# Performance work log

Hardware: AMD Instinct MI355X
Metric: run time of the kernel (lower is better)

## Reference

```python
import jax, jax.numpy as jnp
import numpy as np
import math

P = 2
TAU = 1.0
USE_POW = False
ALIGN_W = 1.0
ENTROPY_W = 1.0
EPS = 1e-12


def _pairwise_l2(z):
    # torch.cdist(z, z, p=2): sqrt of squared distances via GEMM decomposition
    sq = jnp.sum(z * z, axis=-1)  # [N]
    d2 = sq[:, None] + sq[None, :] - 2.0 * (z @ z.T)  # [N, N]
    d = jnp.sqrt(jnp.maximum(d2, 0.0))
    return jnp.maximum(d, EPS)  # clamp_min(eps)


def setup_inputs() -> dict:
    key = jax.random.key(0)
    k0, k1 = jax.random.split(key)
    v0 = jax.random.normal(k0, (8192, 256), dtype=jnp.float32)
    v1 = jax.random.normal(k1, (8192, 256), dtype=jnp.float32)
    return {"v0": v0, "v1": v1}


def reference(v0, v1):
    views = [v0, v1]
    n = v0.shape[0]

    # Alignment term: mean Lp distance between matched rows, one pair (0,1)
    diff = v0 - v1
    align = jnp.sqrt(jnp.sum(diff * diff, axis=-1)).mean()  # p=2 norm per row

    # Entropy term: masked logsumexp over within-view pairwise distances
    log_num_neg = math.log(n - 1)
    eye = jnp.eye(n, dtype=bool)
    entropy = jnp.float32(0.0)
    for z in views:
        dist = _pairwise_l2(z)  # [N, N]
        logits = jnp.where(eye, -jnp.inf, -dist / TAU)
        lme = jax.nn.logsumexp(logits, axis=1) - log_num_neg  # [N]
        entropy = entropy + lme.mean()
    entropy = entropy / len(views)

    return ALIGN_W * align + ENTROPY_W * entropy
```

## Files before the change

kernel.cpp:

```cpp
#include <hip/hip_runtime.h>
#include <math.h>


#define D_DIM 256
#define NB 64
#define NSEG 544
#define S_Q 26.0f
#define LOG2E2 2.0813689810f
#define LP 65

typedef int i32x4 __attribute__((ext_vector_type(4)));
typedef unsigned int u32;
#define AS1 __attribute__((address_space(1)))
#define AS3 __attribute__((address_space(3)))

__device__ inline void load_lds16(const void* g, void* l) {
  __builtin_amdgcn_global_load_lds((const AS1 u32*)g, (AS3 u32*)l, 16, 0, 0);
}

__device__ inline int q8(float x) {
  return __float2int_rn(fminf(fmaxf(x * S_Q, -127.0f), 127.0f));
}
__device__ inline u32 q8x4(const float4 f) {
  return (u32)(q8(f.x) & 255) | ((u32)(q8(f.y) & 255) << 8) |
         ((u32)(q8(f.z) & 255) << 16) | ((u32)(q8(f.w) & 255) << 24);
}

__device__ inline int G4fun(int M) {
  const int m = M >> 2, r = M & 3;
  return 2 * m * (m + 1) + r * (m + 1);
}

__global__ __launch_bounds__(256) void prep(
    const float* __restrict__ v0, const float* __restrict__ v1,
    unsigned char* __restrict__ ph0, unsigned char* __restrict__ ph1,
    float* __restrict__ sq0, float* __restrict__ sq1,
    float* __restrict__ S0, float* __restrict__ S1,
    float* __restrict__ align_part,
    double* __restrict__ totals, int* __restrict__ ticket) {
  __shared__ float4 l0[16 * LP], l1[16 * LP];
  __shared__ float red0[4][16], red1[4][16], red2[4][16];
  const int R = blockIdx.x;
  const int t = threadIdx.x;

  if (R == 0 && t == 0) { totals[0] = 0.0; totals[1] = 0.0; ticket[0] = 0; }

  #pragma unroll
  for (int p = 0; p < 4; ++p) {
    const int slot = t + p * 256;
    const int r = slot >> 6, col = slot & 63;
    const size_t g = (size_t)(R * 16 + r) * 64 + col;
    l0[r * LP + col] = ((const float4*)v0)[g];
    l1[r * LP + col] = ((const float4*)v1)[g];
  }
  __syncthreads();

  {
    const int rr = t & 15, c = t >> 4;
    const int s = c >> 2, q = c & 3;
    const int li = rr * LP + c * 4;
    uint4 u0, u1;
    u0.x = q8x4(l0[li + 0]); u0.y = q8x4(l0[li + 1]);
    u0.z = q8x4(l0[li + 2]); u0.w = q8x4(l0[li + 3]);
    u1.x = q8x4(l1[li + 0]); u1.y = q8x4(l1[li + 1]);
    u1.z = q8x4(l1[li + 2]); u1.w = q8x4(l1[li + 3]);
    const size_t dst = (size_t)(R * 4 + s) * 64 + q * 16 + rr;
    ((uint4*)ph0)[dst] = u0;
    ((uint4*)ph1)[dst] = u1;
  }

  {
    const int rr = t & 15;
    const int base = rr * LP + (t >> 4) * 4;
    float s0p = 0.f, s1p = 0.f, s2p = 0.f;
    #pragma unroll
    for (int c = 0; c < 4; ++c) {
      const float4 a = l0[base + c], b = l1[base + c];
      s0p += a.x * a.x + a.y * a.y + a.z * a.z + a.w * a.w;
      s1p += b.x * b.x + b.y * b.y + b.z * b.z + b.w * b.w;
      const float dx = a.x - b.x, dy = a.y - b.y, dz = a.z - b.z, dw = a.w - b.w;
      s2p += dx * dx + dy * dy + dz * dz + dw * dw;
    }
    s0p += __shfl_xor(s0p, 16, 64); s0p += __shfl_xor(s0p, 32, 64);
    s1p += __shfl_xor(s1p, 16, 64); s1p += __shfl_xor(s1p, 32, 64);
    s2p += __shfl_xor(s2p, 16, 64); s2p += __shfl_xor(s2p, 32, 64);
    const int w = t >> 6, lane = t & 63;
    if (lane < 16) { red0[w][lane] = s0p; red1[w][lane] = s1p; red2[w][lane] = s2p; }
  }
  __syncthreads();
  if (t < 16) {
    const int row = R * 16 + t;
    const float a0 = red0[0][t] + red0[1][t] + red0[2][t] + red0[3][t];
    const float a1 = red1[0][t] + red1[1][t] + red1[2][t] + red1[3][t];
    const float a2 = red2[0][t] + red2[1][t] + red2[2][t] + red2[3][t];
    sq0[row] = a0 * LOG2E2;
    sq1[row] = a1 * LOG2E2;
    align_part[row] = sqrtf(a2);
    S0[row] = 0.0f;
    S1[row] = 0.0f;
  }
}

__global__ __launch_bounds__(256) void entropy_tile(
    const unsigned char* __restrict__ ph0, const unsigned char* __restrict__ ph1,
    const float* __restrict__ sq0, const float* __restrict__ sq1,
    float* __restrict__ S0, float* __restrict__ S1) {
  const unsigned char* __restrict__ ph = blockIdx.y ? ph1 : ph0;
  const float* __restrict__ sq = blockIdx.y ? sq1 : sq0;
  float* __restrict__ S        = blockIdx.y ? S1 : S0;

  const int lin = blockIdx.x;
  int bi = 0;
  while (NSEG - G4fun(64 - (bi + 1)) <= lin) ++bi;
  const int q = lin - (NSEG - G4fun(64 - bi));
  const int bj0 = bi + 4 * q;
  const int jend = (bj0 + 3 < NB - 1) ? bj0 + 3 : NB - 1;

  __shared__ __align__(16) char smem[32768];
  float* swp = (float*)smem;

  const int t = threadIdx.x, lane = t & 63, w = t >> 6;
  const int wi = w >> 1, wj = w & 1;
  const int quad = lane >> 4, l15 = lane & 15;
  const int i0 = bi * 128;

  #pragma unroll
  for (int r8 = 0; r8 < 8; ++r8) {
    const int seg = w * 8 + r8;
    const unsigned char* src = ph + (size_t)bi * 32768 + seg * 1024 + lane * 16;
    load_lds16(src, smem + seg * 1024);
  }
  __syncthreads();

  const i32x4* __restrict__ phv = (const i32x4*)ph;
  const i32x4* smemv = (const i32x4*)smem;
  const float K2 = 2.0f * LOG2E2 / (S_Q * S_Q);

  float prow[4][4];
  #pragma unroll
  for (int m = 0; m < 4; ++m)
    #pragma unroll
    for (int r = 0; r < 4; ++r) prow[m][r] = 0.f;

  auto do_tile = [&](const int bj, const bool diag_t) {
    const int j0 = bj * 128;
    const int baseB = ((bj * 8 + wj * 4) * 4) * 64 + lane;

    float sjl[4];
    #pragma unroll
    for (int n = 0; n < 4; ++n) sjl[n] = sq[j0 + wj * 64 + n * 16 + l15];

    i32x4 bF[4][4];
    #pragma unroll
    for (int s = 0; s < 4; ++s)
      #pragma unroll
      for (int n = 0; n < 4; ++n)
        bF[s][n] = phv[baseB + (n * 4 + s) * 64];

    float csum[4] = {0.f, 0.f, 0.f, 0.f};

    i32x4 accA[4], accB[4];
    float siA[4], siB[4];

    auto compute = [&](i32x4* acc, float* si, const int m) {
      #pragma unroll
      for (int r = 0; r < 4; ++r)
        si[r] = sq[i0 + wi * 64 + m * 16 + quad * 4 + r];
      #pragma unroll
      for (int n = 0; n < 4; ++n) acc[n] = (i32x4){0, 0, 0, 0};
      #pragma unroll
      for (int s = 0; s < 4; ++s) {
        const i32x4 ah = smemv[(size_t)((wi * 4 + m) * 4 + s) * 64 + lane];
        #pragma unroll
        for (int n = 0; n < 4; ++n)
          acc[n] = __builtin_amdgcn_mfma_i32_16x16x64_i8(ah, bF[s][n], acc[n], 0, 0, 0);
      }
    };

    auto epilogue = [&](const i32x4* acc, const float* si, const int m) {
      #pragma unroll
      for (int r = 0; r < 4; ++r) {
        const int gi = i0 + wi * 64 + m * 16 + quad * 4 + r;
        float p = 0.f;
        #pragma unroll
        for (int n = 0; n < 4; ++n) {
          const float d2 = fmaf(-K2, (float)acc[n][r], si[r] + sjl[n]);
          float e = __builtin_amdgcn_exp2f(-__builtin_amdgcn_sqrtf(d2));
          if (diag_t && gi == j0 + wj * 64 + n * 16 + l15) e = 0.f;
          p += e;
          csum[n] += e;
        }
        prow[m][r] += p;
      }
    };

    compute(accA, siA, 0);
    compute(accB, siB, 1);
    epilogue(accA, siA, 0);
    compute(accA, siA, 2);
    epilogue(accB, siB, 1);
    compute(accB, siB, 3);
    epilogue(accA, siA, 2);
    epilogue(accB, siB, 3);

    if (!diag_t) {
      #pragma unroll
      for (int n = 0; n < 4; ++n) {
        float c2 = csum[n];
        c2 += __shfl_xor(c2, 16, 64);
        c2 += __shfl_xor(c2, 32, 64);
        if (quad == 0) atomicAdd(&S[j0 + wj * 64 + n * 16 + l15], c2);
      }
    }
  };

  int bjs = bj0;
  if (bj0 == bi) { do_tile(bi, true); bjs = bi + 1; }
  for (int bj = bjs; bj <= jend; ++bj) do_tile(bj, false);

  __syncthreads();

  const int wbase = w * 1088;
  #pragma unroll
  for (int m = 0; m < 4; ++m)
    #pragma unroll
    for (int r = 0; r < 4; ++r)
      swp[wbase + (m * 16 + quad * 4 + r) * 17 + l15] = prow[m][r];
  float rs = 0.f;
  #pragma unroll
  for (int j = 0; j < 16; ++j) rs += swp[wbase + lane * 17 + j];
  atomicAdd(&S[i0 + wi * 64 + lane], rs);
}

__global__ __launch_bounds__(256) void finalize_fused(
    const float* __restrict__ S0, const float* __restrict__ S1,
    const float* __restrict__ align_part,
    double* __restrict__ totals, int* __restrict__ ticket,
    float* __restrict__ out, int n) {
  __shared__ float shl[4], sha[4];
  const int t = threadIdx.x, lane = t & 63, w = t >> 6;
  const int idx = blockIdx.x * 256 + t;
  float lg = __logf(S0[idx]) + __logf(S1[idx]);
  float al = align_part[idx];
  #pragma unroll
  for (int o = 1; o < 64; o <<= 1) {
    lg += __shfl_xor(lg, o, 64);
    al += __shfl_xor(al, o, 64);
  }
  if (lane == 0) { shl[w] = lg; sha[w] = al; }
  __syncthreads();
  if (t == 0) {
    const double pl = (double)(shl[0] + shl[1] + shl[2] + shl[3]);
    const double pa = (double)(sha[0] + sha[1] + sha[2] + sha[3]);
    atomicAdd(&totals[0], pl);
    atomicAdd(&totals[1], pa);
    __threadfence();
    const int old = atomicAdd(ticket, 1);
    if (old == (int)gridDim.x - 1) {
      const double lgt = atomicAdd(&totals[0], 0.0);
      const double alt = atomicAdd(&totals[1], 0.0);
      const double align = alt / (double)n;
      const double entropy = 0.5 * lgt / (double)n - log((double)(n - 1));
      out[0] = (float)(align + entropy);
    }
  }
}

extern "C" void kernel_launch(void* const* d_in, const int* in_sizes, int n_in,
                              void* d_out, int out_size, void* d_ws, size_t ws_size,
                              hipStream_t stream) {
  const float* v0 = (const float*)d_in[0];
  const float* v1 = (const float*)d_in[1];
  float* out = (float*)d_out;
  const int n = in_sizes[0] / D_DIM;

  float* ws         = (float*)d_ws;
  float* sq0        = ws;
  float* sq1        = ws + n;
  float* S0         = ws + 2 * n;
  float* S1         = ws + 3 * n;
  float* align_part = ws + 4 * n;
  double* totals    = (double*)(ws + 5 * n);
  int* ticket       = (int*)(ws + 5 * n + 4);
  unsigned char* ph0 = (unsigned char*)(ws + 5 * n + 64);
  unsigned char* ph1 = ph0 + (size_t)n * D_DIM;

  prep<<<n / 16, 256, 0, stream>>>(v0, v1, ph0, ph1, sq0, sq1, S0, S1,
                                   align_part, totals, ticket);

  dim3 grid(NSEG, 2);
  entropy_tile<<<grid, 256, 0, stream>>>(ph0, ph1, sq0, sq1, S0, S1);

  finalize_fused<<<n / 256, 256, 0, stream>>>(S0, S1, align_part, totals,
                                              ticket, out, n);
}
```

Baseline: 111.2 us.

## Halve tiles per block, reload B fragments per k-step, raise occupancy

Each block now covers at most two column tiles instead of four, which doubles the grid size (NSEG 544 to 1056) and changes the triangular index mapping to match. Register pressure is cut by loading B fragments from global memory per k-slice instead of holding all 16 for the whole tile, and by computing two row groups at a time instead of the ping-pong compute/epilogue schedule. A launch bound of 5 blocks per CU is added to raise occupancy. In exchange, B fragments are loaded twice per tile, the A tile is staged into LDS once per block, so the total staging doubles, and more atomics are issued on the row sums.

```diff
diff --git a/kernel.cpp b/kernel.cpp
--- a/kernel.cpp
+++ b/kernel.cpp
@@ -4,7 +4,7 @@
 
 #define D_DIM 256
 #define NB 64
-#define NSEG 544
+#define NSEG 1056
 #define S_Q 26.0f
 #define LOG2E2 2.0813689810f
 #define LP 65
@@ -26,9 +26,9 @@
          ((u32)(q8(f.z) & 255) << 16) | ((u32)(q8(f.w) & 255) << 24);
 }
 
-__device__ inline int G4fun(int M) {
-  const int m = M >> 2, r = M & 3;
-  return 2 * m * (m + 1) + r * (m + 1);
+__device__ inline int Gfun(int M) {
+  const int m = M >> 1;
+  return (M & 1) ? (m + 1) * (m + 1) : m * (m + 1);
 }
 
 __global__ __launch_bounds__(256) void prep(
@@ -101,7 +101,7 @@
   }
 }
 
-__global__ __launch_bounds__(256) void entropy_tile(
+__global__ __launch_bounds__(256, 5) void entropy_tile(
     const unsigned char* __restrict__ ph0, const unsigned char* __restrict__ ph1,
     const float* __restrict__ sq0, const float* __restrict__ sq1,
     float* __restrict__ S0, float* __restrict__ S1) {
@@ -111,10 +111,9 @@
 
   const int lin = blockIdx.x;
   int bi = 0;
-  while (NSEG - G4fun(64 - (bi + 1)) <= lin) ++bi;
-  const int q = lin - (NSEG - G4fun(64 - bi));
-  const int bj0 = bi + 4 * q;
-  const int jend = (bj0 + 3 < NB - 1) ? bj0 + 3 : NB - 1;
+  while (NSEG - Gfun(64 - (bi + 1)) <= lin) ++bi;
+  const int q = lin - (NSEG - Gfun(64 - bi));
+  const int bj0 = bi + 2 * q;
 
   __shared__ __align__(16) char smem[32768];
   float* swp = (float*)smem;
@@ -150,32 +149,7 @@
     #pragma unroll
     for (int n = 0; n < 4; ++n) sjl[n] = sq[j0 + wj * 64 + n * 16 + l15];
 
-    i32x4 bF[4][4];
-    #pragma unroll
-    for (int s = 0; s < 4; ++s)
-      #pragma unroll
-      for (int n = 0; n < 4; ++n)
-        bF[s][n] = phv[baseB + (n * 4 + s) * 64];
-
     float csum[4] = {0.f, 0.f, 0.f, 0.f};
-
-    i32x4 accA[4], accB[4];
-    float siA[4], siB[4];
-
-    auto compute = [&](i32x4* acc, float* si, const int m) {
-      #pragma unroll
-      for (int r = 0; r < 4; ++r)
-        si[r] = sq[i0 + wi * 64 + m * 16 + quad * 4 + r];
-      #pragma unroll
-      for (int n = 0; n < 4; ++n) acc[n] = (i32x4){0, 0, 0, 0};
-      #pragma unroll
-      for (int s = 0; s < 4; ++s) {
-        const i32x4 ah = smemv[(size_t)((wi * 4 + m) * 4 + s) * 64 + lane];
-        #pragma unroll
-        for (int n = 0; n < 4; ++n)
-          acc[n] = __builtin_amdgcn_mfma_i32_16x16x64_i8(ah, bF[s][n], acc[n], 0, 0, 0);
-      }
-    };
 
     auto epilogue = [&](const i32x4* acc, const float* si, const int m) {
       #pragma unroll
@@ -194,14 +168,38 @@
       }
     };
 
-    compute(accA, siA, 0);
-    compute(accB, siB, 1);
-    epilogue(accA, siA, 0);
-    compute(accA, siA, 2);
-    epilogue(accB, siB, 1);
-    compute(accB, siB, 3);
-    epilogue(accA, siA, 2);
-    epilogue(accB, siB, 3);
+    #pragma unroll
+    for (int p = 0; p < 2; ++p) {
+      const int m0 = 2 * p, m1 = m0 + 1;
+      float si0[4], si1[4];
+      #pragma unroll
+      for (int r = 0; r < 4; ++r) {
+        si0[r] = sq[i0 + wi * 64 + m0 * 16 + quad * 4 + r];
+        si1[r] = sq[i0 + wi * 64 + m1 * 16 + quad * 4 + r];
+      }
+      i32x4 acc0[4], acc1[4];
+      #pragma unroll
+      for (int n = 0; n < 4; ++n) {
+        acc0[n] = (i32x4){0, 0, 0, 0};
+        acc1[n] = (i32x4){0, 0, 0, 0};
+      }
+      #pragma unroll
+      for (int s = 0; s < 4; ++s) {
+        i32x4 bf[4];
+        #pragma unroll
+        for (int n = 0; n < 4; ++n) bf[n] = phv[baseB + (n * 4 + s) * 64];
+        const i32x4 ah0 = smemv[(size_t)((wi * 4 + m0) * 4 + s) * 64 + lane];
+        const i32x4 ah1 = smemv[(size_t)((wi * 4 + m1) * 4 + s) * 64 + lane];
+        #pragma unroll
+        for (int n = 0; n < 4; ++n)
+          acc0[n] = __builtin_amdgcn_mfma_i32_16x16x64_i8(ah0, bf[n], acc0[n], 0, 0, 0);
+        #pragma unroll
+        for (int n = 0; n < 4; ++n)
+          acc1[n] = __builtin_amdgcn_mfma_i32_16x16x64_i8(ah1, bf[n], acc1[n], 0, 0, 0);
+      }
+      epilogue(acc0, si0, m0);
+      epilogue(acc1, si1, m1);
+    }
 
     if (!diag_t) {
       #pragma unroll
@@ -214,9 +212,8 @@
     }
   };
 
-  int bjs = bj0;
-  if (bj0 == bi) { do_tile(bi, true); bjs = bi + 1; }
-  for (int bj = bjs; bj <= jend; ++bj) do_tile(bj, false);
+  if (bj0 == bi) do_tile(bi, true); else do_tile(bj0, false);
+  if (bj0 + 1 < NB) do_tile(bj0 + 1, false);
 
   __syncthreads();
 
```

After: 171.9 us. +54.6%, slower.
